# Optimization experiments

Hardware: AMD Instinct MI355X
Metric: run time of the kernel (lower is better)

## Reference

```python
import jax, jax.numpy as jnp
import numpy as np

B, NC, H, GH = 64, 21, 32, 64  # batch, num_class, hidden spatial, geo spatial
DN = ('NCHW', 'OIHW', 'NCHW')


def conv2d(x, w, b, stride, pad):
    y = jax.lax.conv_general_dilated(x, w, (stride, stride), [(pad, pad), (pad, pad)], dimension_numbers=DN)
    return y + b[None, :, None, None]


def group_norm(x, scale, bias, groups=32, eps=1e-5):
    b, c, h, w = x.shape
    xg = x.reshape(b, groups, c // groups, h, w)
    mean = xg.mean(axis=(2, 3, 4), keepdims=True)
    var = xg.var(axis=(2, 3, 4), keepdims=True)
    xn = ((xg - mean) * jax.lax.rsqrt(var + eps)).reshape(b, c, h, w)
    return xn * scale[None, :, None, None] + bias[None, :, None, None]


def setup_inputs() -> dict:
    key = jax.random.key(0)
    ks = iter(jax.random.split(key, 64))
    rn = lambda shape, s=0.05: jax.random.normal(next(ks), shape, jnp.float32) * s
    inp = {
        'hidden_state': jnp.tanh(rn((B, 128, H, H), 1.0)),
        'delta_flow': rn((B, 2, H, H), 1.0),
        'mask': jax.random.uniform(next(ks), (B, 1, H, H), jnp.float32),
        'geo': rn((B, 8, GH, GH), 1.0),
        'obj_id': jax.random.randint(next(ks), (B,), 1, NC + 1),
        # geo_model
        'g1_w': rn((128, 8, 3, 3)), 'g1_b': rn((128,)),
        'g2_w': rn((64, 128, 3, 3)), 'g2_b': rn((64,)),
        # delta_flow_model
        'd1_w': rn((128, 2, 7, 7)), 'd1_b': rn((128,)),
        'd2_w': rn((64, 128, 3, 3)), 'd2_b': rn((64,)),
        # mask_model
        'm1_w': rn((64, 1, 3, 3)), 'm1_b': rn((64,)),
        'm2_w': rn((32, 64, 3, 3)), 'm2_b': rn((32,)),
        # conv_layers (conv + GroupNorm(32) x3, all stride 2)
        'c1_w': rn((128, 288, 3, 3)), 'c1_b': rn((128,)), 'gn1_s': jnp.ones((128,)), 'gn1_bb': jnp.zeros((128,)),
        'c2_w': rn((128, 128, 3, 3)), 'c2_b': rn((128,)), 'gn2_s': jnp.ones((128,)), 'gn2_bb': jnp.zeros((128,)),
        'c3_w': rn((128, 128, 3, 3)), 'c3_b': rn((128,)), 'gn3_s': jnp.ones((128,)), 'gn3_bb': jnp.zeros((128,)),
        # fc_layers
        'fc1_w': rn((1024, 2048)), 'fc1_b': rn((1024,)),
        'fc2_w': rn((256, 1024)), 'fc2_b': rn((256,)),
        # prediction heads (random instead of zero-init so grads are non-trivial)
        'rot_w': rn((6 * NC, 256)), 'rot_b': jnp.tile(jnp.array([1., 0., 0., 0., 1., 0.], jnp.float32), NC),
        'tr_w': rn((3 * NC, 256)), 'tr_b': rn((3 * NC,)),
    }
    return inp


def reference(hidden_state, delta_flow, mask, geo, obj_id,
              g1_w, g1_b, g2_w, g2_b, d1_w, d1_b, d2_w, d2_b, m1_w, m1_b, m2_w, m2_b,
              c1_w, c1_b, gn1_s, gn1_bb, c2_w, c2_b, gn2_s, gn2_bb, c3_w, c3_b, gn3_s, gn3_bb,
              fc1_w, fc1_b, fc2_w, fc2_b, rot_w, rot_b, tr_w, tr_b):
    relu = jax.nn.relu
    geo_enc = relu(conv2d(relu(conv2d(geo, g1_w, g1_b, 1, 1)), g2_w, g2_b, 2, 1))        # [B,64,32,32]
    df_enc = relu(conv2d(relu(conv2d(delta_flow, d1_w, d1_b, 1, 3)), d2_w, d2_b, 1, 1))  # [B,64,32,32]
    m_enc = relu(conv2d(relu(conv2d(mask, m1_w, m1_b, 1, 1)), m2_w, m2_b, 1, 1))         # [B,32,32,32]
    enc = jnp.concatenate([hidden_state, df_enc, m_enc, geo_enc], axis=1)                # [B,288,32,32]
    x = relu(group_norm(conv2d(enc, c1_w, c1_b, 2, 1), gn1_s, gn1_bb))                   # [B,128,16,16]
    x = relu(group_norm(conv2d(x, c2_w, c2_b, 2, 1), gn2_s, gn2_bb))                     # [B,128,8,8]
    x = relu(group_norm(conv2d(x, c3_w, c3_b, 2, 1), gn3_s, gn3_bb))                     # [B,128,4,4]
    x = x.reshape(x.shape[0], -1)                                                        # [B,2048]
    x = relu(x @ fc1_w.T + fc1_b)
    x = relu(x @ fc2_w.T + fc2_b)                                                        # [B,256]
    tr = (x @ tr_w.T + tr_b).reshape(-1, NC, 3)
    rot = (x @ rot_w.T + rot_b).reshape(-1, NC, 6)
    # torch.index_select(., dim=1, index=obj_id-1)[:, 0, :] -> uses obj_id[0]
    tr = jnp.take(tr, obj_id - 1, axis=1)[:, 0, :]
    rot = jnp.take(rot, obj_id - 1, axis=1)[:, 0, :]
    return (rot, tr)
```

## Files before the change

kernel.cpp:

```cpp
#include <hip/hip_runtime.h>
#include <hip/hip_bf16.h>

typedef __bf16 bf16x8 __attribute__((ext_vector_type(8)));
typedef __bf16 bf16x4 __attribute__((ext_vector_type(4)));
typedef float  f32x4  __attribute__((ext_vector_type(4)));

struct PackArgs {
    const float* src[11];
    __bf16* dst[11];
    int Cout[11], Cin[11], KHW[11], KW[11], Cinpad[11], Kpad[11], mode[11];
    int cum[12];
};

__device__ void pack_dev(const PackArgs& pa, int gidx)
{
    if (gidx >= pa.cum[11]) return;
    int s = 0;
    for (int i = 1; i <= 10; ++i) s += (gidx >= pa.cum[i]) ? 1 : 0;
    int l = gidx - pa.cum[s];
    int Kp = pa.Kpad[s];
    int co = l / Kp, k = l - co * Kp;
    float v = 0.f;
    if (co < pa.Cout[s]) {
        if (pa.mode[s] == 0) {
            int cip = pa.Cinpad[s];
            int tap = k / cip, ci = k - tap * cip;
            if (tap < pa.KHW[s] && ci < pa.Cin[s])
                v = pa.src[s][((long)co * pa.Cin[s] + ci) * pa.KHW[s] + tap];
        } else if (pa.mode[s] == 1) {
            int pix = k >> 7, c = k & 127;
            v = pa.src[s][(long)co * 2048 + c * 16 + pix];
        } else if (pa.mode[s] == 2) {
            v = pa.src[s][(long)co * Kp + k];
        } else {
            int kh = k >> 4, r = k & 15, kw = r >> 1, ci = r & 1;
            if (kh < 7 && kw < 7)
                v = pa.src[s][((long)(co * 2 + ci) * 7 + kh) * 7 + kw];
        }
    }
    pa.dst[s][l] = (__bf16)v;
}

struct BulkPack { const float* s[8]; __bf16* d[8]; };

template<int CO, int CIN, int KP>
__device__ __forceinline__ void pack_conv8(const float* __restrict__ src,
                                           __bf16* __restrict__ dst, int eb)
{
    int e = eb * 8;
    int co = e / KP;
    int k  = e - co * KP;
    int tap = k / CIN;
    int ci  = k - tap * CIN;
    bf16x8 o = {};
    if (co < CO && tap < 9) {
        const float* s = src + ((long)co * CIN + ci) * 9 + tap;
#pragma unroll
        for (int j = 0; j < 8; ++j) o[j] = (__bf16)s[j * 9];
    }
    *(bf16x8*)&dst[e] = o;
}

__device__ __forceinline__ void pack_fc1_8(const float* __restrict__ src,
                                           __bf16* __restrict__ dst, int eb)
{
    int e = eb * 8;
    int co = e >> 11, k = e & 2047;
    int pix = k >> 7, c = k & 127;
    const float* s = src + (long)co * 2048 + c * 16 + pix;
    bf16x8 o;
#pragma unroll
    for (int j = 0; j < 8; ++j) o[j] = (__bf16)s[j * 16];
    *(bf16x8*)&dst[e] = o;
}

__device__ __forceinline__ void pack_fc2_8(const float* __restrict__ src,
                                           __bf16* __restrict__ dst, int eb)
{
    int e = eb * 8;
    f32x4 lo = *(const f32x4*)&src[e];
    f32x4 hi = *(const f32x4*)&src[e + 4];
    bf16x8 o = { (__bf16)lo.x, (__bf16)lo.y, (__bf16)lo.z, (__bf16)lo.w,
                 (__bf16)hi.x, (__bf16)hi.y, (__bf16)hi.z, (__bf16)hi.w };
    *(bf16x8*)&dst[e] = o;
}

__device__ void pad_nhwc8v_dev(const float* __restrict__ in, __bf16* __restrict__ out,
                               int C, int log2HW, int pidx)
{
    int b = pidx >> log2HW;
    int pix = pidx & ((1 << log2HW) - 1);
    const float* s = in + (((long)b * C) << log2HW) + pix;
    bf16x8 o = {};
    for (int c = 0; c < C; ++c) o[c] = (__bf16)s[(long)c << log2HW];
    *(bf16x8*)&out[(long)pidx * 8] = o;
}

__device__ void pad_dflow_dev(const float* __restrict__ in, __bf16* __restrict__ out, int idx)
{
    if (idx >= 64 * 40 * 40 * 2) return;
    int c = idx & 1;
    int t = idx >> 1;
    int x = t % 40;
    int t2 = t / 40;
    int y = t2 % 40;
    int b = t2 / 40;
    int hi = y - 3, wi = x - 3;
    float v = 0.f;
    if ((unsigned)hi < 32u && (unsigned)wi < 32u)
        v = in[((long)(b * 2 + c) * 32 + hi) * 32 + wi];
    out[idx] = (__bf16)v;
}

__device__ void hid_dev(char* smem, const float* __restrict__ h,
                        __bf16* __restrict__ enc, int blk, int tid)
{
    auto t = reinterpret_cast<float (*)[65]>(smem);
    int b = blk >> 6;
    int inner = blk & 63;
    int ct = inner & 3, pt = inner >> 2;
    int c0 = ct * 32, p0 = pt * 64;
    int cl = tid >> 6, pl = tid & 63;
#pragma unroll
    for (int i = 0; i < 8; ++i)
        t[cl + i * 4][pl] = h[((long)(b * 128 + c0 + cl + i * 4)) * 1024 + p0 + pl];
    __syncthreads();
    int cc = tid & 31, p2 = tid >> 5;
#pragma unroll
    for (int i = 0; i < 8; ++i)
        enc[((long)b * 1024 + p0 + p2 + i * 8) * 288 + c0 + cc] = (__bf16)t[cc][p2 + i * 8];
}

#define PACK_B 144
#define GEOV_B 1024
#define DF_B 800
#define MASKV_B 256
#define ZERO_B 80
__global__ __launch_bounds__(256) void prep_kern(PackArgs pa,
    const float* __restrict__ geo, __bf16* __restrict__ geo_p,
    const float* __restrict__ dflow, __bf16* __restrict__ dflow_pp,
    const float* __restrict__ mask, __bf16* __restrict__ mask_p,
    float* __restrict__ fc1acc, float* __restrict__ fc2acc)
{
    int blk = blockIdx.x, tid = threadIdx.x;
    if (blk < PACK_B) { pack_dev(pa, blk * 256 + tid); return; }
    blk -= PACK_B;
    if (blk < GEOV_B) { pad_nhwc8v_dev(geo, geo_p, 8, 12, blk * 256 + tid); return; }
    blk -= GEOV_B;
    if (blk < DF_B) { pad_dflow_dev(dflow, dflow_pp, blk * 256 + tid); return; }
    blk -= DF_B;
    if (blk < MASKV_B) { pad_nhwc8v_dev(mask, mask_p, 1, 10, blk * 256 + tid); return; }
    blk -= MASKV_B;
    long zi = (long)blk * 256 + tid;
    f32x4 z = {};
    if (zi < 16384) *(f32x4*)&fc1acc[zi * 4] = z;
    else { zi -= 16384; *(f32x4*)&fc2acc[zi * 4] = z; }
}

struct ConvGeom {
    int CinTot;
    int Hin, Win;
    int log2HWout, log2Wout;
    int stride, pad;
    int Kpad;
    int KHW;
    int Cout, CTOT, C0;
    int b0i, b0o;
};

template<int BM, int BN, int BK, int THREADS, int WMW, int WNW, int CINPAD, int KW, int MODE, bool OUTBF, bool RELU>
__device__ __forceinline__ void conv_dev2(char* __restrict__ smem_, int bx,
    const __bf16* __restrict__ in_, const __bf16* __restrict__ A,
    const float* __restrict__ bias, void* __restrict__ out_, const ConvGeom& g)
{
    constexpr int MEXT = BM / WMW;
    constexpr int NEXT = BN / WNW;
    constexpr int MFRAG = MEXT / 16;
    constexpr int NFRAG = NEXT / 16;
    constexpr int KROW = BK / 8;
    constexpr int SROWS = THREADS / KROW;
    constexpr int APASS = BM / SROWS;
    constexpr int BPASS = BN / SROWS;
    constexpr int LDK = BK + 8;

    auto As = reinterpret_cast<__bf16 (*)[LDK]>(smem_);
    auto Bs = reinterpret_cast<__bf16 (*)[LDK]>(smem_ + (size_t)BM * LDK * sizeof(__bf16));

    const int tid = threadIdx.x;
    const int ntile = bx * BN;
    const int lane = tid & 63, w = tid >> 6;
    const int wm = (w / WNW) * MEXT, wn = (w % WNW) * NEXT;
    const int lr = lane & 15, lk = (lane >> 4) * 8;
    const int srow = tid / KROW, scol = (tid % KROW) * 8;

    long nbase[BPASS]; int hi0a[BPASS], wi0a[BPASS];
#pragma unroll
    for (int j = 0; j < BPASS; ++j) {
        int n = ntile + j * SROWS + srow;
        int bb = g.b0i + (n >> g.log2HWout);
        int pix = n & ((1 << g.log2HWout) - 1);
        int ho = pix >> g.log2Wout, wo = pix & ((1 << g.log2Wout) - 1);
        hi0a[j] = ho * g.stride - g.pad;
        wi0a[j] = wo * g.stride - g.pad;
        nbase[j] = (((long)bb * g.Hin + hi0a[j]) * g.Win + wi0a[j]) * g.CinTot;
    }

    bf16x8 av[APASS], bv[BPASS];
    auto LOAD = [&](int k0) {
        int k = k0 + scol;
#pragma unroll
        for (int ja = 0; ja < APASS; ++ja)
            av[ja] = *(const bf16x8*)&A[(long)(ja * SROWS + srow) * g.Kpad + k];
        if (MODE == 1) {
            int q = k >> 3;
            int off = (q >> 1) * (g.Win * g.CinTot) + (q & 1) * 8;
#pragma unroll
            for (int j = 0; j < BPASS; ++j)
                bv[j] = *(const bf16x8*)&in_[nbase[j] + off];
        } else {
            int tap = k / CINPAD;
            int ci  = k - tap * CINPAD;
            int kh  = tap / KW;
            int kw  = tap - kh * KW;
            bool tv = tap < g.KHW;
            int off = (kh * g.Win + kw) * g.CinTot + ci;
#pragma unroll
            for (int j = 0; j < BPASS; ++j) {
                bf16x8 z = {};
                int hi = hi0a[j] + kh, wi = wi0a[j] + kw;
                if (tv && (unsigned)hi < (unsigned)g.Hin && (unsigned)wi < (unsigned)g.Win)
                    z = *(const bf16x8*)&in_[nbase[j] + off];
                bv[j] = z;
            }
        }
    };

    f32x4 acc[MFRAG][NFRAG] = {};
    LOAD(0);
    for (int k0 = 0;;) {
        if (k0) __syncthreads();
#pragma unroll
        for (int ja = 0; ja < APASS; ++ja)
            *(bf16x8*)&As[ja * SROWS + srow][scol] = av[ja];
#pragma unroll
        for (int j = 0; j < BPASS; ++j)
            *(bf16x8*)&Bs[j * SROWS + srow][scol] = bv[j];
        __syncthreads();
        int kn = k0 + BK;
        bool more = kn < g.Kpad;
        if (more) LOAD(kn);
#pragma unroll
        for (int kk = 0; kk < BK; kk += 32) {
            bf16x8 bfr[NFRAG], afr[MFRAG];
#pragma unroll
            for (int jn = 0; jn < NFRAG; ++jn)
                bfr[jn] = *(const bf16x8*)&Bs[wn + jn * 16 + lr][kk + lk];
#pragma unroll
            for (int i = 0; i < MFRAG; ++i)
                afr[i] = *(const bf16x8*)&As[wm + i * 16 + lr][kk + lk];
#pragma unroll
            for (int i = 0; i < MFRAG; ++i)
#pragma unroll
                for (int jn = 0; jn < NFRAG; ++jn)
                    acc[i][jn] = __builtin_amdgcn_mfma_f32_16x16x32_bf16(afr[i], bfr[jn], acc[i][jn], 0, 0, 0);
        }
        if (!more) break;
        k0 = kn;
    }

    const int HWm1 = (1 << g.log2HWout) - 1;
#pragma unroll
    for (int i = 0; i < MFRAG; ++i) {
        int co = wm + i * 16 + (lane >> 4) * 4;
        if (co >= g.Cout) continue;
        f32x4 bv4 = *(const f32x4*)&bias[co];
#pragma unroll
        for (int jn = 0; jn < NFRAG; ++jn) {
            int nn = ntile + wn + jn * 16 + lr;
            f32x4 v = acc[i][jn] + bv4;
            if (RELU) { v.x = fmaxf(v.x, 0.f); v.y = fmaxf(v.y, 0.f); v.z = fmaxf(v.z, 0.f); v.w = fmaxf(v.w, 0.f); }
            int ob = nn >> g.log2HWout, opix = nn & HWm1;
            long o = (((long)(g.b0o + ob) << g.log2HWout) + opix) * g.CTOT + g.C0 + co;
            if (OUTBF) {
                bf16x4 o4 = { (__bf16)v.x, (__bf16)v.y, (__bf16)v.z, (__bf16)v.w };
                *(bf16x4*)&((__bf16*)out_)[o] = o4;
            } else {
                *(f32x4*)&((float*)out_)[o] = v;
            }
        }
    }
}

template<int BM, int BN, int BK, int THREADS, int CINPAD, int KW, int MODE, bool OUTBF, bool RELU>
__device__ __forceinline__ void conv_dev(char* __restrict__ smem_, int bx,
    const __bf16* __restrict__ in_, const __bf16* __restrict__ A,
    const float* __restrict__ bias, void* __restrict__ out_, const ConvGeom& g)
{
    constexpr int WAVES = THREADS / 64;
    constexpr int WN = BN / 32;
    constexpr int WM = WAVES / WN;
    constexpr int MEXT = BM / WM;
    constexpr int MFRAG = MEXT / 16;
    constexpr int KROW = BK / 8;
    constexpr int SROWS = THREADS / KROW;
    constexpr int APASS = BM / SROWS;
    constexpr int BPASS = BN / SROWS;

    auto As = reinterpret_cast<__bf16 (*)[BK + 8]>(smem_);
    auto Bs = reinterpret_cast<__bf16 (*)[BK + 8]>(smem_ + (size_t)BM * (BK + 8) * sizeof(__bf16));

    const int tid = threadIdx.x;
    const int ntile = bx * BN;
    const int lane = tid & 63, w = tid >> 6;
    const int wm = (w / WN) * MEXT, wn = (w % WN) * 32;
    const int lr = lane & 15, lk = (lane >> 4) * 8;
    const int srow = tid / KROW, scol = (tid % KROW) * 8;

    long nbase[BPASS]; int hi0a[BPASS], wi0a[BPASS];
#pragma unroll
    for (int j = 0; j < BPASS; ++j) {
        int n = ntile + j * SROWS + srow;
        int bb = g.b0i + (n >> g.log2HWout);
        int pix = n & ((1 << g.log2HWout) - 1);
        int ho = pix >> g.log2Wout, wo = pix & ((1 << g.log2Wout) - 1);
        hi0a[j] = ho * g.stride - g.pad;
        wi0a[j] = wo * g.stride - g.pad;
        nbase[j] = (((long)bb * g.Hin + hi0a[j]) * g.Win + wi0a[j]) * g.CinTot;
    }

    bf16x8 av[APASS], bv[BPASS];
    auto LOAD = [&](int k0) {
        int k = k0 + scol;
#pragma unroll
        for (int ja = 0; ja < APASS; ++ja)
            av[ja] = *(const bf16x8*)&A[(long)(ja * SROWS + srow) * g.Kpad + k];
        if (MODE == 1) {
            int q = k >> 3;
            int off = (q >> 1) * (g.Win * g.CinTot) + (q & 1) * 8;
#pragma unroll
            for (int j = 0; j < BPASS; ++j)
                bv[j] = *(const bf16x8*)&in_[nbase[j] + off];
        } else {
            int tap = k / CINPAD;
            int ci  = k - tap * CINPAD;
            int kh  = tap / KW;
            int kw  = tap - kh * KW;
            bool tv = tap < g.KHW;
            int off = (kh * g.Win + kw) * g.CinTot + ci;
#pragma unroll
            for (int j = 0; j < BPASS; ++j) {
                bf16x8 z = {};
                int hi = hi0a[j] + kh, wi = wi0a[j] + kw;
                if (tv && (unsigned)hi < (unsigned)g.Hin && (unsigned)wi < (unsigned)g.Win)
                    z = *(const bf16x8*)&in_[nbase[j] + off];
                bv[j] = z;
            }
        }
    };

    f32x4 acc[MFRAG][2] = {};
    LOAD(0);
    for (int k0 = 0;;) {
        if (k0) __syncthreads();
#pragma unroll
        for (int ja = 0; ja < APASS; ++ja)
            *(bf16x8*)&As[ja * SROWS + srow][scol] = av[ja];
#pragma unroll
        for (int j = 0; j < BPASS; ++j)
            *(bf16x8*)&Bs[j * SROWS + srow][scol] = bv[j];
        __syncthreads();
        int kn = k0 + BK;
        bool more = kn < g.Kpad;
        if (more) LOAD(kn);
#pragma unroll
        for (int kk = 0; kk < BK; kk += 32) {
            bf16x8 bfr[2];
            bfr[0] = *(const bf16x8*)&Bs[wn + lr][kk + lk];
            bfr[1] = *(const bf16x8*)&Bs[wn + 16 + lr][kk + lk];
#pragma unroll
            for (int i = 0; i < MFRAG; ++i) {
                bf16x8 a = *(const bf16x8*)&As[wm + i * 16 + lr][kk + lk];
                acc[i][0] = __builtin_amdgcn_mfma_f32_16x16x32_bf16(a, bfr[0], acc[i][0], 0, 0, 0);
                acc[i][1] = __builtin_amdgcn_mfma_f32_16x16x32_bf16(a, bfr[1], acc[i][1], 0, 0, 0);
            }
        }
        if (!more) break;
        k0 = kn;
    }

    const int HWm1 = (1 << g.log2HWout) - 1;
#pragma unroll
    for (int i = 0; i < MFRAG; ++i) {
        int co = wm + i * 16 + (lane >> 4) * 4;
        if (co >= g.Cout) continue;
        f32x4 bv4 = *(const f32x4*)&bias[co];
#pragma unroll
        for (int jb = 0; jb < 2; ++jb) {
            int nn = ntile + wn + jb * 16 + lr;
            f32x4 v = acc[i][jb] + bv4;
            if (RELU) { v.x = fmaxf(v.x, 0.f); v.y = fmaxf(v.y, 0.f); v.z = fmaxf(v.z, 0.f); v.w = fmaxf(v.w, 0.f); }
            int ob = nn >> g.log2HWout, opix = nn & HWm1;
            long o = (((long)(g.b0o + ob) << g.log2HWout) + opix) * g.CTOT + g.C0 + co;
            if (OUTBF) {
                bf16x4 o4 = { (__bf16)v.x, (__bf16)v.y, (__bf16)v.z, (__bf16)v.w };
                *(bf16x4*)&((__bf16*)out_)[o] = o4;
            } else {
                *(f32x4*)&((float*)out_)[o] = v;
            }
        }
    }
}

template<int BM, int BN, int BK, int THREADS, int WMW, int WNW, int CINPAD, int KW, int MODE, bool OUTBF, bool RELU>
__global__ __launch_bounds__(THREADS) void conv_gemm2(
    const __bf16* __restrict__ in_, const __bf16* __restrict__ A,
    const float* __restrict__ bias, void* __restrict__ out_, ConvGeom g)
{
    __shared__ __attribute__((aligned(16))) char smem[(BM + BN) * (BK + 8) * 2];
    int mt = blockIdx.y * BM;
    ConvGeom gg = g;
    gg.C0 += mt;
    gg.Cout -= mt;
    conv_dev2<BM, BN, BK, THREADS, WMW, WNW, CINPAD, KW, MODE, OUTBF, RELU>(
        smem, blockIdx.x, in_, A + (long)mt * g.Kpad, bias + mt, out_, gg);
}

template<int BM, int BN, int BK, int THREADS, int WMW, int WNW, int CINPAD, int KW, int PPB>
__global__ __launch_bounds__(THREADS) void conv_gn_kern(
    const __bf16* __restrict__ in_, const __bf16* __restrict__ A,
    const float* __restrict__ bias, const float* __restrict__ gns,
    const float* __restrict__ gnb, __bf16* __restrict__ out_, ConvGeom g)
{
    constexpr int MEXT = BM / WMW;
    constexpr int NEXT = BN / WNW;
    constexpr int MFRAG = MEXT / 16;
    constexpr int NFRAG = NEXT / 16;
    constexpr int KROW = BK / 8;
    constexpr int SROWS = THREADS / KROW;
    constexpr int APASS = BM / SROWS;
    constexpr int BPASS = BN / SROWS;
    constexpr int LDK = BK + 8;

    __shared__ __attribute__((aligned(16))) char smem_[(BM + BN) * (BK + 8) * 2];
    auto As = reinterpret_cast<__bf16 (*)[LDK]>(smem_);
    auto Bs = reinterpret_cast<__bf16 (*)[LDK]>(smem_ + (size_t)BM * LDK * sizeof(__bf16));
    static_assert((size_t)BN * (BM + 4) * 4 <= (size_t)(BM + BN) * (BK + 8) * 2, "smf fits");

    const int tid = threadIdx.x;
    const int mt = blockIdx.y * BM;
    const __bf16* Ap = A + (long)mt * g.Kpad;
    const int C0 = g.C0 + mt;
    const int ntile = blockIdx.x * BN;
    const int lane = tid & 63, w = tid >> 6;
    const int wm = (w / WNW) * MEXT, wn = (w % WNW) * NEXT;
    const int lr = lane & 15, lk = (lane >> 4) * 8;
    const int srow = tid / KROW, scol = (tid % KROW) * 8;

    long nbase[BPASS]; int hi0a[BPASS], wi0a[BPASS];
#pragma unroll
    for (int j = 0; j < BPASS; ++j) {
        int n = ntile + j * SROWS + srow;
        int bb = g.b0i + (n >> g.log2HWout);
        int pix = n & ((1 << g.log2HWout) - 1);
        int ho = pix >> g.log2Wout, wo = pix & ((1 << g.log2Wout) - 1);
        hi0a[j] = ho * g.stride - g.pad;
        wi0a[j] = wo * g.stride - g.pad;
        nbase[j] = (((long)bb * g.Hin + hi0a[j]) * g.Win + wi0a[j]) * g.CinTot;
    }

    bf16x8 av[APASS], bv[BPASS];
    auto LOAD = [&](int k0) {
        int k = k0 + scol;
#pragma unroll
        for (int ja = 0; ja < APASS; ++ja)
            av[ja] = *(const bf16x8*)&Ap[(long)(ja * SROWS + srow) * g.Kpad + k];
        int tap = k / CINPAD;
        int ci  = k - tap * CINPAD;
        int kh  = tap / KW;
        int kw  = tap - kh * KW;
        bool tv = tap < g.KHW;
        int off = (kh * g.Win + kw) * g.CinTot + ci;
#pragma unroll
        for (int j = 0; j < BPASS; ++j) {
            bf16x8 z = {};
            int hi = hi0a[j] + kh, wi = wi0a[j] + kw;
            if (tv && (unsigned)hi < (unsigned)g.Hin && (unsigned)wi < (unsigned)g.Win)
                z = *(const bf16x8*)&in_[nbase[j] + off];
            bv[j] = z;
        }
    };

    f32x4 acc[MFRAG][NFRAG] = {};
    LOAD(0);
    for (int k0 = 0;;) {
        if (k0) __syncthreads();
#pragma unroll
        for (int ja = 0; ja < APASS; ++ja)
            *(bf16x8*)&As[ja * SROWS + srow][scol] = av[ja];
#pragma unroll
        for (int j = 0; j < BPASS; ++j)
            *(bf16x8*)&Bs[j * SROWS + srow][scol] = bv[j];
        __syncthreads();
        int kn = k0 + BK;
        bool more = kn < g.Kpad;
        if (more) LOAD(kn);
#pragma unroll
        for (int kk = 0; kk < BK; kk += 32) {
            bf16x8 bfr[NFRAG], afr[MFRAG];
#pragma unroll
            for (int jn = 0; jn < NFRAG; ++jn)
                bfr[jn] = *(const bf16x8*)&Bs[wn + jn * 16 + lr][kk + lk];
#pragma unroll
            for (int i = 0; i < MFRAG; ++i)
                afr[i] = *(const bf16x8*)&As[wm + i * 16 + lr][kk + lk];
#pragma unroll
            for (int i = 0; i < MFRAG; ++i)
#pragma unroll
                for (int jn = 0; jn < NFRAG; ++jn)
                    acc[i][jn] = __builtin_amdgcn_mfma_f32_16x16x32_bf16(afr[i], bfr[jn], acc[i][jn], 0, 0, 0);
        }
        if (!more) break;
        k0 = kn;
    }

    __syncthreads();
    auto smf = reinterpret_cast<float (*)[BM + 4]>(smem_);
#pragma unroll
    for (int i = 0; i < MFRAG; ++i) {
        int m = wm + i * 16 + (lane >> 4) * 4;
        f32x4 bv4 = *(const f32x4*)&bias[C0 + m];
#pragma unroll
        for (int jn = 0; jn < NFRAG; ++jn) {
            int n = wn + jn * 16 + lr;
            *(f32x4*)&smf[n][m] = acc[i][jn] + bv4;
        }
    }
    __syncthreads();

    constexpr int NSETS = (BN / PPB) * (BM / 4);
    constexpr int TPS = THREADS / NSETS;
    constexpr int PPT = PPB / TPS;
    const int set = tid / TPS, part = tid % TPS;
    const int bit = set / (BM / 4);
    const int grp = set % (BM / 4);
    const int m0 = grp * 4;
    float sum = 0.f, sq = 0.f;
#pragma unroll
    for (int p = 0; p < PPT; ++p) {
        int nl = bit * PPB + part + p * TPS;
        f32x4 v = *(const f32x4*)&smf[nl][m0];
        sum += v.x + v.y + v.z + v.w;
        sq  += v.x * v.x + v.y * v.y + v.z * v.z + v.w * v.w;
    }
#pragma unroll
    for (int off = TPS >> 1; off > 0; off >>= 1) {
        sum += __shfl_xor(sum, off);
        sq  += __shfl_xor(sq, off);
    }
    const float len = (float)(PPB * 4);
    float mean = sum / len;
    float var  = sq / len - mean * mean;
    float rstd = rsqrtf(fmaxf(var, 0.f) + 1e-5f);
    f32x4 s4 = *(const f32x4*)&gns[C0 + m0];
    f32x4 b4 = *(const f32x4*)&gnb[C0 + m0];
    const int HWm1 = (1 << g.log2HWout) - 1;
#pragma unroll
    for (int p = 0; p < PPT; ++p) {
        int nl = bit * PPB + part + p * TPS;
        f32x4 v = *(const f32x4*)&smf[nl][m0];
        f32x4 r;
        r.x = fmaxf((v.x - mean) * rstd * s4.x + b4.x, 0.f);
        r.y = fmaxf((v.y - mean) * rstd * s4.y + b4.y, 0.f);
        r.z = fmaxf((v.z - mean) * rstd * s4.z + b4.z, 0.f);
        r.w = fmaxf((v.w - mean) * rstd * s4.w + b4.w, 0.f);
        int n = ntile + nl;
        int ob = n >> g.log2HWout, opix = n & HWm1;
        long o = (((long)(g.b0o + ob) << g.log2HWout) + opix) * g.CTOT + C0 + m0;
        bf16x4 o4 = { (__bf16)r.x, (__bf16)r.y, (__bf16)r.z, (__bf16)r.w };
        *(bf16x4*)&out_[o] = o4;
    }
}

#define B1_CONV 3072
#define B1_PACK 775
__global__ __launch_bounds__(512) void branch1_kern(
    const __bf16* __restrict__ geo_p, const __bf16* __restrict__ wg1, const float* __restrict__ g1_b, __bf16* __restrict__ g1out,
    const __bf16* __restrict__ dflow_pp, const __bf16* __restrict__ wd1, const float* __restrict__ d1_b, __bf16* __restrict__ d1out,
    const __bf16* __restrict__ mask_p, const __bf16* __restrict__ wm1, const float* __restrict__ m1_b, __bf16* __restrict__ m1out,
    BulkPack bp, ConvGeom gg1, ConvGeom gd1, ConvGeom gm1)
{
    __shared__ __attribute__((aligned(16))) char smem[27648];
    int x = blockIdx.x;
    if (x < 2048) {
        conv_dev<128, 128, 32, 512, 8, 3, 0, true, true>(smem, x, geo_p, wg1, g1_b, g1out, gg1);
        return;
    }
    if (x < 2560) {
        conv_dev<128, 128, 32, 512, 8, 7, 1, true, true>(smem, x - 2048, dflow_pp, wd1, d1_b, d1out, gd1);
        return;
    }
    if (x < B1_CONV) {
        conv_dev<64, 128, 64, 512, 8, 3, 0, true, true>(smem, x - 2560, mask_p, wm1, m1_b, m1out, gm1);
        return;
    }
    int x2 = x - B1_CONV;
    int tid = threadIdx.x;
    if (x2 < 18)       pack_conv8<64, 128, 1152>(bp.s[0], bp.d[0], x2 * 512 + tid);
    else if (x2 < 36)  pack_conv8<64, 128, 1152>(bp.s[1], bp.d[1], (x2 - 18) * 512 + tid);
    else if (x2 < 45)  pack_conv8<32, 64, 576>(bp.s[2], bp.d[2], (x2 - 36) * 512 + tid);
    else if (x2 < 127) pack_conv8<128, 288, 2624>(bp.s[3], bp.d[3], (x2 - 45) * 512 + tid);
    else if (x2 < 163) pack_conv8<128, 128, 1152>(bp.s[4], bp.d[4], (x2 - 127) * 512 + tid);
    else if (x2 < 199) pack_conv8<128, 128, 1152>(bp.s[5], bp.d[5], (x2 - 163) * 512 + tid);
    else if (x2 < 711) pack_fc1_8(bp.s[6], bp.d[6], (x2 - 199) * 512 + tid);
    else               pack_fc2_8(bp.s[7], bp.d[7], (x2 - 711) * 512 + tid);
}

#define B2_CONV 1536
#define B2_HID 4096
__global__ __launch_bounds__(256) void branch2_kern(
    const __bf16* __restrict__ g1out, const __bf16* __restrict__ wg2, const float* __restrict__ g2_b,
    const __bf16* __restrict__ d1out, const __bf16* __restrict__ wd2, const float* __restrict__ d2_b,
    const __bf16* __restrict__ m1out, const __bf16* __restrict__ wm2, const float* __restrict__ m2_b,
    const float* __restrict__ hidden, __bf16* __restrict__ enc,
    ConvGeom gg2, ConvGeom gd2, ConvGeom gm2)
{
    __shared__ __attribute__((aligned(16))) char smem[(64 + 128) * (64 + 8) * 2];
    int x = blockIdx.x;
    if (x >= B2_CONV) { hid_dev(smem, hidden, enc, x - B2_CONV, threadIdx.x); return; }
    int sec = x % 3, bx = x / 3;
    if (sec == 0)
        conv_dev2<64, 128, 64, 256, 1, 4, 128, 3, 0, true, true>(smem, bx, g1out, wg2, g2_b, enc, gg2);
    else if (sec == 1)
        conv_dev2<64, 128, 64, 256, 1, 4, 128, 3, 0, true, true>(smem, bx, d1out, wd2, d2_b, enc, gd2);
    else
        conv_dev2<64, 128, 64, 256, 1, 4, 64, 3, 0, true, true>(smem, bx, m1out, wm2, m2_b, enc, gm2);
}

__global__ __launch_bounds__(256) void fc1_splitk(
    const __bf16* __restrict__ A, const __bf16* __restrict__ B,
    float* __restrict__ outacc)
{
    __shared__ __attribute__((aligned(16))) __bf16 As[64][40];
    __shared__ __attribute__((aligned(16))) __bf16 Bs[64][40];
    const int tid = threadIdx.x;
    const int mtile = blockIdx.y * 64;
    const int kbase = blockIdx.x * 512;
    const int lane = tid & 63, w = tid >> 6;
    const int wm = (w >> 1) * 32, wn = (w & 1) * 32;
    const int lr = lane & 15, lk = (lane >> 4) * 8;
    const int srow = tid >> 2, soff = (tid & 3) * 8;

    f32x4 acc00 = {}, acc01 = {}, acc10 = {}, acc11 = {};
    for (int k0 = 0; k0 < 512; k0 += 32) {
        *(bf16x8*)&As[srow][soff] = *(const bf16x8*)&A[(long)(mtile + srow) * 2048 + kbase + k0 + soff];
        *(bf16x8*)&Bs[srow][soff] = *(const bf16x8*)&B[(long)srow * 2048 + kbase + k0 + soff];
        __syncthreads();
        bf16x8 a0 = *(const bf16x8*)&As[wm + lr][lk];
        bf16x8 a1 = *(const bf16x8*)&As[wm + 16 + lr][lk];
        bf16x8 b0f = *(const bf16x8*)&Bs[wn + lr][lk];
        bf16x8 b1f = *(const bf16x8*)&Bs[wn + 16 + lr][lk];
        acc00 = __builtin_amdgcn_mfma_f32_16x16x32_bf16(a0, b0f, acc00, 0, 0, 0);
        acc01 = __builtin_amdgcn_mfma_f32_16x16x32_bf16(a0, b1f, acc01, 0, 0, 0);
        acc10 = __builtin_amdgcn_mfma_f32_16x16x32_bf16(a1, b0f, acc10, 0, 0, 0);
        acc11 = __builtin_amdgcn_mfma_f32_16x16x32_bf16(a1, b1f, acc11, 0, 0, 0);
        __syncthreads();
    }
    f32x4 accs[2][2] = { { acc00, acc01 }, { acc10, acc11 } };
#pragma unroll
    for (int mi = 0; mi < 2; ++mi) {
        int co0 = mtile + wm + mi * 16 + (lane >> 4) * 4;
#pragma unroll
        for (int ni = 0; ni < 2; ++ni) {
            int nn = wn + ni * 16 + lr;
            f32x4 v = accs[mi][ni];
            float* dst = &outacc[(long)nn * 1024 + co0];
            atomicAdd(dst + 0, v.x);
            atomicAdd(dst + 1, v.y);
            atomicAdd(dst + 2, v.z);
            atomicAdd(dst + 3, v.w);
        }
    }
}

__global__ __launch_bounds__(256) void fc2_splitk(
    const __bf16* __restrict__ A, const float* __restrict__ Bacc,
    const float* __restrict__ bb, float* __restrict__ outacc)
{
    __shared__ __attribute__((aligned(16))) __bf16 As[64][40];
    __shared__ __attribute__((aligned(16))) __bf16 Bs[64][40];
    const int tid = threadIdx.x;
    const int mtile = blockIdx.y * 64;
    const int kbase = blockIdx.x * 256;
    const int lane = tid & 63, w = tid >> 6;
    const int wm = (w >> 1) * 32, wn = (w & 1) * 32;
    const int lr = lane & 15, lk = (lane >> 4) * 8;
    const int srow = tid >> 2, soff = (tid & 3) * 8;

    f32x4 acc00 = {}, acc01 = {}, acc10 = {}, acc11 = {};
    for (int k0 = 0; k0 < 256; k0 += 32) {
        int k = kbase + k0 + soff;
        *(bf16x8*)&As[srow][soff] = *(const bf16x8*)&A[(long)(mtile + srow) * 1024 + k];
        f32x4 lo = *(const f32x4*)&Bacc[(long)srow * 1024 + k];
        f32x4 hi = *(const f32x4*)&Bacc[(long)srow * 1024 + k + 4];
        f32x4 blo = *(const f32x4*)&bb[k];
        f32x4 bhi = *(const f32x4*)&bb[k + 4];
        bf16x8 bvv;
        bvv[0] = (__bf16)fmaxf(lo.x + blo.x, 0.f);
        bvv[1] = (__bf16)fmaxf(lo.y + blo.y, 0.f);
        bvv[2] = (__bf16)fmaxf(lo.z + blo.z, 0.f);
        bvv[3] = (__bf16)fmaxf(lo.w + blo.w, 0.f);
        bvv[4] = (__bf16)fmaxf(hi.x + bhi.x, 0.f);
        bvv[5] = (__bf16)fmaxf(hi.y + bhi.y, 0.f);
        bvv[6] = (__bf16)fmaxf(hi.z + bhi.z, 0.f);
        bvv[7] = (__bf16)fmaxf(hi.w + bhi.w, 0.f);
        *(bf16x8*)&Bs[srow][soff] = bvv;
        __syncthreads();
        bf16x8 a0 = *(const bf16x8*)&As[wm + lr][lk];
        bf16x8 a1 = *(const bf16x8*)&As[wm + 16 + lr][lk];
        bf16x8 b0f = *(const bf16x8*)&Bs[wn + lr][lk];
        bf16x8 b1f = *(const bf16x8*)&Bs[wn + 16 + lr][lk];
        acc00 = __builtin_amdgcn_mfma_f32_16x16x32_bf16(a0, b0f, acc00, 0, 0, 0);
        acc01 = __builtin_amdgcn_mfma_f32_16x16x32_bf16(a0, b1f, acc01, 0, 0, 0);
        acc10 = __builtin_amdgcn_mfma_f32_16x16x32_bf16(a1, b0f, acc10, 0, 0, 0);
        acc11 = __builtin_amdgcn_mfma_f32_16x16x32_bf16(a1, b1f, acc11, 0, 0, 0);
        __syncthreads();
    }
    f32x4 accs[2][2] = { { acc00, acc01 }, { acc10, acc11 } };
#pragma unroll
    for (int mi = 0; mi < 2; ++mi) {
        int co0 = mtile + wm + mi * 16 + (lane >> 4) * 4;
#pragma unroll
        for (int ni = 0; ni < 2; ++ni) {
            int nn = wn + ni * 16 + lr;
            f32x4 v = accs[mi][ni];
            float* dst = &outacc[(long)nn * 256 + co0];
            atomicAdd(dst + 0, v.x);
            atomicAdd(dst + 1, v.y);
            atomicAdd(dst + 2, v.z);
            atomicAdd(dst + 3, v.w);
        }
    }
}

__global__ void gn_nhwc(const float* __restrict__ in, const float* __restrict__ s,
                        const float* __restrict__ bi, __bf16* __restrict__ out,
                        int C, int HW)
{
    int b = blockIdx.x >> 5, g = blockIdx.x & 31;
    int tid = threadIdx.x, nt = blockDim.x;
    const float* p = in + (long)b * HW * C + g * 4;
    float sum = 0.f, sq = 0.f;
    for (int i = tid; i < HW; i += nt) {
        f32x4 v = *(const f32x4*)&p[(long)i * C];
        sum += v.x + v.y + v.z + v.w;
        sq  += v.x * v.x + v.y * v.y + v.z * v.z + v.w * v.w;
    }
    __shared__ float rs[256], rq[256];
    rs[tid] = sum; rq[tid] = sq; __syncthreads();
    for (int off = nt >> 1; off > 0; off >>= 1) {
        if (tid < off) { rs[tid] += rs[tid + off]; rq[tid] += rq[tid + off]; }
        __syncthreads();
    }
    int len = HW * 4;
    float mean = rs[0] / len;
    float var  = rq[0] / len - mean * mean;
    float rstd = rsqrtf(fmaxf(var, 0.f) + 1e-5f);
    f32x4 s4 = *(const f32x4*)&s[g * 4];
    f32x4 b4 = *(const f32x4*)&bi[g * 4];
    __bf16* q = out + (long)b * HW * C + g * 4;
    for (int i = tid; i < HW; i += nt) {
        f32x4 v = *(const f32x4*)&p[(long)i * C];
        f32x4 r;
        r.x = fmaxf((v.x - mean) * rstd * s4.x + b4.x, 0.f);
        r.y = fmaxf((v.y - mean) * rstd * s4.y + b4.y, 0.f);
        r.z = fmaxf((v.z - mean) * rstd * s4.z + b4.z, 0.f);
        r.w = fmaxf((v.w - mean) * rstd * s4.w + b4.w, 0.f);
        bf16x4 o4 = { (__bf16)r.x, (__bf16)r.y, (__bf16)r.z, (__bf16)r.w };
        *(bf16x4*)&q[(long)i * C] = o4;
    }
}

__global__ __launch_bounds__(576) void head_kern(
    const float* __restrict__ x, const float* __restrict__ fb,
    const float* __restrict__ rw, const float* __restrict__ rb,
    const float* __restrict__ tw, const float* __restrict__ tb,
    const int* __restrict__ obj, float* __restrict__ out)
{
    int b = blockIdx.x;
    int k = threadIdx.x >> 6;
    int lane = threadIdx.x & 63;
    int j = obj[0] - 1;
    const float* xr = x + (long)b * 256;
    const float* wr;
    float bias0;
    if (k < 6) { wr = rw + (long)(j * 6 + k) * 256; bias0 = rb[j * 6 + k]; }
    else       { wr = tw + (long)(j * 3 + (k - 6)) * 256; bias0 = tb[j * 3 + (k - 6)]; }
    float acc = 0.f;
#pragma unroll
    for (int p = 0; p < 4; ++p) {
        int i = lane + p * 64;
        float xv = fmaxf(xr[i] + fb[i], 0.f);
        acc = fmaf(xv, wr[i], acc);
    }
#pragma unroll
    for (int off = 32; off > 0; off >>= 1) acc += __shfl_down(acc, off);
    if (lane == 0) {
        float r = acc + bias0;
        if (k < 6) out[b * 6 + k] = r;
        else       out[384 + b * 3 + (k - 6)] = r;
    }
}

extern "C" void kernel_launch(void* const* d_in, const int* in_sizes, int n_in,
                              void* d_out, int out_size, void* d_ws, size_t ws_size,
                              hipStream_t stream)
{
    const float* hidden = (const float*)d_in[0];
    const float* dflow  = (const float*)d_in[1];
    const float* mask   = (const float*)d_in[2];
    const float* geo    = (const float*)d_in[3];
    const int*   obj    = (const int*)d_in[4];
    const float* g1_w = (const float*)d_in[5],  *g1_b = (const float*)d_in[6];
    const float* g2_w = (const float*)d_in[7],  *g2_b = (const float*)d_in[8];
    const float* d1_w = (const float*)d_in[9],  *d1_b = (const float*)d_in[10];
    const float* d2_w = (const float*)d_in[11], *d2_b = (const float*)d_in[12];
    const float* m1_w = (const float*)d_in[13], *m1_b = (const float*)d_in[14];
    const float* m2_w = (const float*)d_in[15], *m2_b = (const float*)d_in[16];
    const float* c1_w = (const float*)d_in[17], *c1_b = (const float*)d_in[18];
    const float* gn1_s = (const float*)d_in[19], *gn1_bb = (const float*)d_in[20];
    const float* c2_w = (const float*)d_in[21], *c2_b = (const float*)d_in[22];
    const float* gn2_s = (const float*)d_in[23], *gn2_bb = (const float*)d_in[24];
    const float* c3_w = (const float*)d_in[25], *c3_b = (const float*)d_in[26];
    const float* gn3_s = (const float*)d_in[27], *gn3_bb = (const float*)d_in[28];
    const float* fc1_w = (const float*)d_in[29], *fc1_b = (const float*)d_in[30];
    const float* fc2_w = (const float*)d_in[31], *fc2_b = (const float*)d_in[32];
    const float* rot_w = (const float*)d_in[33], *rot_b = (const float*)d_in[34];
    const float* tr_w  = (const float*)d_in[35], *tr_b  = (const float*)d_in[36];

    char* ws = (char*)d_ws;
    __bf16* enc = (__bf16*)ws;
    char* W = ws + 37748736;
    __bf16* wg1  = (__bf16*)(W + 0);
    __bf16* wd1  = (__bf16*)(W + 24576);
    __bf16* wm1  = (__bf16*)(W + 57344);
    __bf16* wg2  = (__bf16*)(W + 73728);
    __bf16* wd2  = (__bf16*)(W + 221184);
    __bf16* wm2  = (__bf16*)(W + 368640);
    __bf16* wc1  = (__bf16*)(W + 442368);
    __bf16* wc2  = (__bf16*)(W + 1114112);
    __bf16* wc3  = (__bf16*)(W + 1409024);
    __bf16* wfc1 = (__bf16*)(W + 1703936);
    __bf16* wfc2 = (__bf16*)(W + 5898240);
    __bf16* geo_p    = (__bf16*)(ws + 44179456);
    __bf16* dflow_pp = (__bf16*)(ws + 48373760);
    __bf16* mask_p   = (__bf16*)(ws + 48783360);
    __bf16* g1out    = (__bf16*)(ws + 49831936);
    __bf16* d1out    = (__bf16*)(ws + 116940800);
    __bf16* m1out    = (__bf16*)(ws + 133718016);
    float*  c1raw    = (float*)(ws + 142106624);
    __bf16* x1       = (__bf16*)(ws + 150495232);
    __bf16* x2       = (__bf16*)(ws + 156786688);
    __bf16* x3       = (__bf16*)(ws + 158359552);
    float*  fc1acc   = (float*)(ws + 158621696);
    float*  fc2acc   = (float*)(ws + 158883840);

    PackArgs pa;
    {
        const float* srcs[11] = { g1_w, d1_w, m1_w, g2_w, d2_w, m2_w, c1_w, c2_w, c3_w, fc1_w, fc2_w };
        __bf16* dsts[11] = { wg1, wd1, wm1, wg2, wd2, wm2, wc1, wc2, wc3, wfc1, wfc2 };
        int Co[11]  = { 128, 128, 64, 64, 64, 32, 128, 128, 128, 1024, 256 };
        int Ci[11]  = { 8, 2, 1, 128, 128, 64, 288, 128, 128, 0, 0 };
        int KH[11]  = { 9, 49, 9, 9, 9, 9, 9, 9, 9, 0, 0 };
        int KWn[11] = { 3, 7, 3, 3, 3, 3, 3, 3, 3, 0, 0 };
        int Cp[11]  = { 8, 8, 8, 128, 128, 64, 288, 128, 128, 0, 0 };
        int Kp[11]  = { 96, 128, 128, 1152, 1152, 576, 2624, 1152, 1152, 2048, 1024 };
        int Mp[11]  = { 128, 128, 64, 64, 64, 64, 128, 128, 128, 1024, 256 };
        int Md[11]  = { 0, 3, 0, 0, 0, 0, 0, 0, 0, 1, 2 };
        int c = 0; pa.cum[0] = 0;
        for (int i = 0; i < 11; ++i) {
            pa.src[i] = srcs[i]; pa.dst[i] = dsts[i];
            pa.Cout[i] = Co[i]; pa.Cin[i] = Ci[i]; pa.KHW[i] = KH[i]; pa.KW[i] = KWn[i];
            pa.Cinpad[i] = Cp[i]; pa.Kpad[i] = Kp[i]; pa.mode[i] = Md[i];
            c += Mp[i] * Kp[i]; pa.cum[i + 1] = c;
        }
    }
    BulkPack bp;
    {
        const float* s[8] = { g2_w, d2_w, m2_w, c1_w, c2_w, c3_w, fc1_w, fc2_w };
        __bf16* d[8] = { wg2, wd2, wm2, wc1, wc2, wc3, wfc1, wfc2 };
        for (int i = 0; i < 8; ++i) { bp.s[i] = s[i]; bp.d[i] = d[i]; }
    }

    {
        int total_blocks = PACK_B + GEOV_B + DF_B + MASKV_B + ZERO_B;
        prep_kern<<<dim3(total_blocks), 256, 0, stream>>>(pa, geo, geo_p, dflow, dflow_pp,
                                                          mask, mask_p, fc1acc, fc2acc);
    }

    {
        ConvGeom gg1 = { 8, 64, 64, 12, 6, 1, 1, 96, 9, 128, 128, 0, 0, 0 };
        ConvGeom gd1 = { 2, 40, 40, 10, 5, 1, 0, 128, 49, 128, 128, 0, 0, 0 };
        ConvGeom gm1 = { 8, 32, 32, 10, 5, 1, 1, 128, 9, 64, 64, 0, 0, 0 };
        branch1_kern<<<dim3(B1_CONV + B1_PACK), 512, 0, stream>>>(geo_p, wg1, g1_b, g1out,
                                                                  dflow_pp, wd1, d1_b, d1out,
                                                                  mask_p, wm1, m1_b, m1out,
                                                                  bp, gg1, gd1, gm1);
    }
    {
        ConvGeom gg2 = { 128, 64, 64, 10, 5, 2, 1, 1152, 9, 64, 288, 224, 0, 0 };
        ConvGeom gd2 = { 128, 32, 32, 10, 5, 1, 1, 1152, 9, 64, 288, 128, 0, 0 };
        ConvGeom gm2 = { 64, 32, 32, 10, 5, 1, 1, 576, 9, 32, 288, 192, 0, 0 };
        branch2_kern<<<dim3(B2_CONV + B2_HID), 256, 0, stream>>>(g1out, wg2, g2_b,
                                                                 d1out, wd2, d2_b,
                                                                 m1out, wm2, m2_b,
                                                                 hidden, enc, gg2, gd2, gm2);
    }

    {
        ConvGeom gc1 = { 288, 32, 32, 8, 4, 2, 1, 2624, 9, 128, 128, 0, 0, 0 };
        conv_gemm2<64, 128, 64, 256, 1, 4, 288, 3, 0, false, false><<<dim3(128, 2), 256, 0, stream>>>(enc, wc1, c1_b, c1raw, gc1);
    }
    gn_nhwc<<<dim3(2048), 256, 0, stream>>>(c1raw, gn1_s, gn1_bb, x1, 128, 256);

    {
        ConvGeom gc2 = { 128, 16, 16, 6, 3, 2, 1, 1152, 9, 128, 128, 0, 0, 0 };
        conv_gn_kern<64, 64, 64, 256, 2, 2, 128, 3, 64><<<dim3(64, 2), 256, 0, stream>>>(
            x1, wc2, c2_b, gn2_s, gn2_bb, x2, gc2);
    }
    {
        ConvGeom gc3 = { 128, 8, 8, 4, 2, 2, 1, 1152, 9, 128, 128, 0, 0, 0 };
        conv_gn_kern<64, 64, 64, 256, 2, 2, 128, 3, 16><<<dim3(16, 2), 256, 0, stream>>>(
            x2, wc3, c3_b, gn3_s, gn3_bb, x3, gc3);
    }

    fc1_splitk<<<dim3(4, 16), 256, 0, stream>>>(wfc1, x3, fc1acc);
    fc2_splitk<<<dim3(4, 4), 256, 0, stream>>>(wfc2, fc1acc, fc1_b, fc2acc);

    head_kern<<<dim3(64), 576, 0, stream>>>(fc2acc, fc2_b, rot_w, rot_b, tr_w, tr_b, obj, (float*)d_out);
}
```

Measured before the change: 205.5 us.

## Load branch2 conv tiles directly into LDS with swizzled layout

Replaces the branch2 conv tile loader with a new conv_dev3 that uses global_load_lds to copy 16-byte chunks straight from global memory into shared memory, skipping the register round trip. It uses an XOR-swizzled LDS layout to avoid bank conflicts. Out-of-bounds padding pixels read from a zeroed workspace buffer, and an extra zeroing block is added in prep_kern to clear it. There is no double buffering, so loads and MFMA work in each step are still serialized by barriers.

```diff
diff --git a/kernel.cpp b/kernel.cpp
--- a/kernel.cpp
+++ b/kernel.cpp
@@ -4,6 +4,12 @@
 typedef __bf16 bf16x8 __attribute__((ext_vector_type(8)));
 typedef __bf16 bf16x4 __attribute__((ext_vector_type(4)));
 typedef float  f32x4  __attribute__((ext_vector_type(4)));
+
+__device__ __forceinline__ void gload16(const void* g, void* l)
+{
+    __builtin_amdgcn_global_load_lds((const __attribute__((address_space(1))) void*)g,
+                                     (__attribute__((address_space(3))) void*)l, 16, 0, 0);
+}
 
 struct PackArgs {
     const float* src[11];
@@ -135,7 +141,7 @@
 #define GEOV_B 1024
 #define DF_B 800
 #define MASKV_B 256
-#define ZERO_B 80
+#define ZERO_B 81
 __global__ __launch_bounds__(256) void prep_kern(PackArgs pa,
     const float* __restrict__ geo, __bf16* __restrict__ geo_p,
     const float* __restrict__ dflow, __bf16* __restrict__ dflow_pp,
@@ -168,6 +174,109 @@
     int b0i, b0o;
 };
 
+template<int CINPAD>
+__device__ __forceinline__ void conv_dev3(char* __restrict__ smem_, int bx,
+    const __bf16* __restrict__ in_, const __bf16* __restrict__ A,
+    const float* __restrict__ bias, __bf16* __restrict__ out_,
+    const ConvGeom& g, const __bf16* __restrict__ zpad)
+{
+    constexpr int BM = 64, BN = 128, BK = 64;
+    constexpr int ABYTES = BM * BK * 2;
+    const int tid = threadIdx.x;
+    const int w4 = tid >> 6, l = tid & 63;
+    const int lane = l;
+    const int wn = w4 * 32;
+    const int lr = lane & 15, lk = (lane >> 4) * 8;
+    const int ntile = bx * BN;
+
+    int rowA[2], colA[2];
+#pragma unroll
+    for (int j = 0; j < 2; ++j) {
+        int X = ((w4 * 2 + j) << 10) + l * 16;
+        rowA[j] = X >> 7;
+        int cb = (X & 127) ^ ((rowA[j] & 7) << 4);
+        colA[j] = cb >> 1;
+    }
+    int rowB[4], colB[4], hi0a[4], wi0a[4];
+    long nbase[4];
+#pragma unroll
+    for (int j = 0; j < 4; ++j) {
+        int X = ((w4 * 4 + j) << 10) + l * 16;
+        rowB[j] = X >> 7;
+        int cb = (X & 127) ^ ((rowB[j] & 7) << 4);
+        colB[j] = cb >> 1;
+        int n = ntile + rowB[j];
+        int bb = g.b0i + (n >> g.log2HWout);
+        int pix = n & ((1 << g.log2HWout) - 1);
+        int ho = pix >> g.log2Wout, wo = pix & ((1 << g.log2Wout) - 1);
+        hi0a[j] = ho * g.stride - g.pad;
+        wi0a[j] = wo * g.stride - g.pad;
+        nbase[j] = (((long)bb * g.Hin + hi0a[j]) * g.Win + wi0a[j]) * g.CinTot;
+    }
+
+    f32x4 acc[4][2] = {};
+    for (int k0 = 0; k0 < g.Kpad; k0 += BK) {
+        if (k0) __syncthreads();
+#pragma unroll
+        for (int j = 0; j < 2; ++j) {
+            const __bf16* ga = A + (long)rowA[j] * g.Kpad + k0 + colA[j];
+            gload16(ga, smem_ + ((w4 * 2 + j) << 10));
+        }
+        int tap = k0 / CINPAD;
+        int ci0 = k0 % CINPAD;
+        int kh = tap / 3, kw = tap - kh * 3;
+        int toff = (kh * g.Win + kw) * g.CinTot + ci0;
+#pragma unroll
+        for (int j = 0; j < 4; ++j) {
+            int hi = hi0a[j] + kh, wi = wi0a[j] + kw;
+            bool v = (unsigned)hi < (unsigned)g.Hin && (unsigned)wi < (unsigned)g.Win;
+            const __bf16* gb = v ? (in_ + nbase[j] + toff + colB[j]) : (zpad + l * 8);
+            gload16(gb, smem_ + ABYTES + ((w4 * 4 + j) << 10));
+        }
+        __syncthreads();
+#pragma unroll
+        for (int kk = 0; kk < BK; kk += 32) {
+            bf16x8 bfr[2], afr[4];
+#pragma unroll
+            for (int jn = 0; jn < 2; ++jn) {
+                int row = wn + jn * 16 + lr;
+                int byte = ABYTES + row * 128 + (((kk + lk) * 2) ^ ((row & 7) << 4));
+                bfr[jn] = *(const bf16x8*)(smem_ + byte);
+            }
+#pragma unroll
+            for (int i = 0; i < 4; ++i) {
+                int row = i * 16 + lr;
+                int byte = row * 128 + (((kk + lk) * 2) ^ ((row & 7) << 4));
+                afr[i] = *(const bf16x8*)(smem_ + byte);
+            }
+#pragma unroll
+            for (int i = 0; i < 4; ++i) {
+                acc[i][0] = __builtin_amdgcn_mfma_f32_16x16x32_bf16(afr[i], bfr[0], acc[i][0], 0, 0, 0);
+                acc[i][1] = __builtin_amdgcn_mfma_f32_16x16x32_bf16(afr[i], bfr[1], acc[i][1], 0, 0, 0);
+            }
+        }
+    }
+
+    const int HWm1 = (1 << g.log2HWout) - 1;
+#pragma unroll
+    for (int i = 0; i < 4; ++i) {
+        int co = i * 16 + (lane >> 4) * 4;
+        if (co >= g.Cout) continue;
+        f32x4 bv4 = *(const f32x4*)&bias[co];
+#pragma unroll
+        for (int jn = 0; jn < 2; ++jn) {
+            int nn = ntile + wn + jn * 16 + lr;
+            f32x4 v = acc[i][jn] + bv4;
+            v.x = fmaxf(v.x, 0.f); v.y = fmaxf(v.y, 0.f);
+            v.z = fmaxf(v.z, 0.f); v.w = fmaxf(v.w, 0.f);
+            int ob = nn >> g.log2HWout, opix = nn & HWm1;
+            long o = (((long)(g.b0o + ob) << g.log2HWout) + opix) * g.CTOT + g.C0 + co;
+            bf16x4 o4 = { (__bf16)v.x, (__bf16)v.y, (__bf16)v.z, (__bf16)v.w };
+            *(bf16x4*)&out_[o] = o4;
+        }
+    }
+}
+
 template<int BM, int BN, int BK, int THREADS, int WMW, int WNW, int CINPAD, int KW, int MODE, bool OUTBF, bool RELU>
 __device__ __forceinline__ void conv_dev2(char* __restrict__ smem_, int bx,
     const __bf16* __restrict__ in_, const __bf16* __restrict__ A,
@@ -621,19 +730,19 @@
     const __bf16* __restrict__ g1out, const __bf16* __restrict__ wg2, const float* __restrict__ g2_b,
     const __bf16* __restrict__ d1out, const __bf16* __restrict__ wd2, const float* __restrict__ d2_b,
     const __bf16* __restrict__ m1out, const __bf16* __restrict__ wm2, const float* __restrict__ m2_b,
-    const float* __restrict__ hidden, __bf16* __restrict__ enc,
+    const float* __restrict__ hidden, __bf16* __restrict__ enc, const __bf16* __restrict__ zpad,
     ConvGeom gg2, ConvGeom gd2, ConvGeom gm2)
 {
-    __shared__ __attribute__((aligned(16))) char smem[(64 + 128) * (64 + 8) * 2];
+    __shared__ __attribute__((aligned(16))) char smem[24576];
     int x = blockIdx.x;
     if (x >= B2_CONV) { hid_dev(smem, hidden, enc, x - B2_CONV, threadIdx.x); return; }
     int sec = x % 3, bx = x / 3;
     if (sec == 0)
-        conv_dev2<64, 128, 64, 256, 1, 4, 128, 3, 0, true, true>(smem, bx, g1out, wg2, g2_b, enc, gg2);
+        conv_dev3<128>(smem, bx, g1out, wg2, g2_b, enc, gg2, zpad);
     else if (sec == 1)
-        conv_dev2<64, 128, 64, 256, 1, 4, 128, 3, 0, true, true>(smem, bx, d1out, wd2, d2_b, enc, gd2);
+        conv_dev3<128>(smem, bx, d1out, wd2, d2_b, enc, gd2, zpad);
     else
-        conv_dev2<64, 128, 64, 256, 1, 4, 64, 3, 0, true, true>(smem, bx, m1out, wm2, m2_b, enc, gm2);
+        conv_dev3<64>(smem, bx, m1out, wm2, m2_b, enc, gm2, zpad);
 }
 
 __global__ __launch_bounds__(256) void fc1_splitk(
@@ -863,6 +972,7 @@
     __bf16* x3       = (__bf16*)(ws + 158359552);
     float*  fc1acc   = (float*)(ws + 158621696);
     float*  fc2acc   = (float*)(ws + 158883840);
+    __bf16* zpad     = (__bf16*)(ws + 158949376);
 
     PackArgs pa;
     {
@@ -913,7 +1023,8 @@
         branch2_kern<<<dim3(B2_CONV + B2_HID), 256, 0, stream>>>(g1out, wg2, g2_b,
                                                                  d1out, wd2, d2_b,
                                                                  m1out, wm2, m2_b,
-                                                                 hidden, enc, gg2, gd2, gm2);
+                                                                 hidden, enc, zpad,
+                                                                 gg2, gd2, gm2);
     }
 
     {
```

After: 208.9 us. No clear change (+1.6%).
